# Kernel optimization log

Measured on AMD Instinct MI355X. Metric: run time of the kernel, lower is better.

The kernel has to match this reference:

```python
import jax, jax.numpy as jnp
import numpy as np

B, O, D = 4096, 256, 256  # batch, size_out (rules), size_in (features)


def setup_inputs() -> dict:
    key = jax.random.key(0)
    k1, k2, k3, k4, k5 = jax.random.split(key, 5)
    return {
        "x": jax.random.normal(k1, (B, D), dtype=jnp.float32),
        "scales": jax.random.normal(k2, (O, D), dtype=jnp.float32),
        # strict upper triangle holds the packed rot vectors (original inits them to zeros;
        # small values keep the quadratic form well conditioned)
        "rots": jax.random.normal(k3, (O, D, D), dtype=jnp.float32) * 0.02,
        "centroids": jax.random.normal(k4, (O, D, 1), dtype=jnp.float32),
        "b": jax.random.uniform(k5, (O,), dtype=jnp.float32, minval=0.5, maxval=1.5),
    }


def reference(x, scales, rots, centroids, b):
    # Build symmetric transform A[o] = diag(scales[o]) + triu(rots[o],1) + triu(rots[o],1)^T
    # (equivalent to the loop of diag_embed(r_i, i+1) + mirrored lower diagonal).
    upper = jnp.triu(rots, 1)                                   # [O,D,D]
    A = upper + jnp.swapaxes(upper, -1, -2)
    A = A + jnp.eye(D, dtype=scales.dtype) * scales[:, None, :]  # diag_embed(scales)
    # Augmented affine map: mul[o,i,b'] = A[o] @ x[b'] + centroid[o,i]; const row dropped
    # since only the first size_in rows feed the norm.
    y = jnp.einsum('bj,oij->boi', x, A) + centroids[..., 0][None, :, :]  # [B,O,D]
    rx = jnp.sqrt(jnp.sum(y * y, axis=-1))                      # L2 norm over D -> [B,O]
    return 1.0 / (1.0 + rx ** (2.0 * b))                        # bell membership [B,O]
```

## Files before the change

kernel.cpp:

```cpp
#include <hip/hip_runtime.h>
#include <cstdint>
#include <cmath>

#define Bn 4096
#define Dn 256
#define On 256

typedef __bf16 v8bf __attribute__((ext_vector_type(8)));
typedef float  v16f __attribute__((ext_vector_type(16)));
typedef unsigned short us8 __attribute__((ext_vector_type(8)));

__device__ __forceinline__ unsigned short f2bf(float f) {
    unsigned int u = __builtin_bit_cast(unsigned int, f);
    unsigned int r = (u + 0x7fffu + ((u >> 16) & 1u)) >> 16;
    return (unsigned short)r;
}

__device__ __forceinline__ void gl_lds16(const void* g, void* l) {
    __builtin_amdgcn_global_load_lds(
        (const __attribute__((address_space(1))) void*)(uintptr_t)g,
        (__attribute__((address_space(3))) void*)(uintptr_t)l, 16, 0, 0);
}

__global__ __launch_bounds__(256) void prep_x(const float* __restrict__ x,
                                              unsigned short* __restrict__ xbT) {
    __shared__ float t[64][68];
    const int tid = threadIdx.x;
    const int bb = blockIdx.x >> 2;
    const int kb = blockIdx.x & 3;
    const int b0 = bb * 64;
#pragma unroll
    for (int s = 0; s < 4; ++s) {
        const int idx = s * 256 + tid;
        const int r = idx >> 4, c4 = idx & 15;
        const float4 v = *(const float4*)(x + (size_t)(b0 + r) * Dn + kb * 64 + c4 * 4);
        *(float4*)&t[r][c4 * 4] = v;
    }
    __syncthreads();
    const int lane = tid & 63, wv = tid >> 6;
#pragma unroll
    for (int s = 0; s < 2; ++s) {
        const int kcl = s * 4 + wv;
        us8 u;
#pragma unroll
        for (int q = 0; q < 8; ++q) u[q] = f2bf(t[lane][kcl * 8 + q]);
        *(us8*)(xbT + ((size_t)(kb * 8 + kcl) * Bn + b0 + lane) * 8) = u;
    }
}

template <int TI, int TJ>
__device__ __forceinline__ void extract_pair(const float* T, v8bf (&af)[16],
                                             float sc, int wv, int lane) {
    const int l31 = lane & 31, hw = lane >> 5;
    const int half = wv & 1, grp = wv >> 1;
    if (TI == TJ) {
        if (grp == TI) {
            const int r = half * 32 + l31;
            const int mr = (r & 7) << 2;
#pragma unroll
            for (int kq = 0; kq < 4; ++kq) {
                us8 u;
#pragma unroll
                for (int q = 0; q < 8; ++q) {
                    const int c = kq * 16 + hw * 8 + q;
                    const float v = (r < c) ? T[r * 64 + (c ^ mr)]
                                  : ((r > c) ? T[c * 64 + (r ^ ((c & 7) << 2))]
                                             : sc);
                    u[q] = f2bf(v);
                }
                af[TI * 4 + kq] = __builtin_bit_cast(v8bf, u);
            }
        }
    } else {
        if (grp == TI) {
            const int r = half * 32 + l31;
            const int mr = (r & 7) << 2;
#pragma unroll
            for (int kq = 0; kq < 4; ++kq) {
                const int c0 = kq * 16 + hw * 8;
                const float4 a = *(const float4*)&T[r * 64 + (c0 ^ mr)];
                const float4 b = *(const float4*)&T[r * 64 + ((c0 + 4) ^ mr)];
                us8 u;
                u[0] = f2bf(a.x); u[1] = f2bf(a.y); u[2] = f2bf(a.z); u[3] = f2bf(a.w);
                u[4] = f2bf(b.x); u[5] = f2bf(b.y); u[6] = f2bf(b.z); u[7] = f2bf(b.w);
                af[TJ * 4 + kq] = __builtin_bit_cast(v8bf, u);
            }
        } else if (grp == TJ) {
            const int cL = half * 32 + l31;
#pragma unroll
            for (int kq = 0; kq < 4; ++kq) {
                us8 u;
#pragma unroll
                for (int q = 0; q < 8; ++q) {
                    const int rL = kq * 16 + hw * 8 + q;
                    u[q] = f2bf(T[rL * 64 + (cL ^ ((rL & 7) << 2))]);
                }
                af[TI * 4 + kq] = __builtin_bit_cast(v8bf, u);
            }
        }
    }
}

#define WAITV(N)                                              \
    do {                                                      \
        asm volatile("s_waitcnt vmcnt(" #N ")" ::: "memory"); \
        __builtin_amdgcn_sched_barrier(0);                    \
    } while (0)
#define LGKM0()                                               \
    do {                                                      \
        asm volatile("s_waitcnt lgkmcnt(0)" ::: "memory");    \
        __builtin_amdgcn_sched_barrier(0);                    \
    } while (0)
#define BARF()                                                \
    do {                                                      \
        __builtin_amdgcn_sched_barrier(0);                    \
        __builtin_amdgcn_s_barrier();                         \
        __builtin_amdgcn_sched_barrier(0);                    \
    } while (0)

#define STAGE_T(TIv, TJv, DST)                                               \
    do {                                                                     \
        const float* s_ = rbase + (TIv) * (64 * Dn) + (TJv) * 64;            \
        _Pragma("unroll")                                                    \
        for (int s = 0; s < 2; ++s) {                                        \
            const int idx = s * 512 + tid;                                   \
            const int r = idx >> 4, c4 = idx & 15;                           \
            gl_lds16(s_ + (size_t)r * Dn + ((c4 ^ (r & 7)) * 4),             \
                     (DST) + idx * 4);                                       \
        }                                                                    \
    } while (0)

#define STAGE_X(BUF)                                                         \
    do {                                                                     \
        _Pragma("unroll")                                                    \
        for (int s = 0; s < 2; ++s) {                                        \
            gl_lds16(px[s], &Xs[BUF][s * 512 + tid][0]);                     \
            px[s] += 256;                  \
        }                                                                    \
    } while (0)

__global__ __launch_bounds__(512, 4) void fuzzy_main(
    const float* __restrict__ rots, const float* __restrict__ scales,
    const unsigned short* __restrict__ xbT, const float* __restrict__ cent,
    const float* __restrict__ bvals, float* __restrict__ out) {
    __shared__ __align__(16) unsigned short Xs[4][1024][8];
    __shared__ float ssbuf[2][8][32];
    __shared__ float centL[Dn];

    const int tid  = threadIdx.x;
    const int lane = tid & 63;
    const int wv   = tid >> 6;
    const int l31  = lane & 31, hw = lane >> 5;
    const int Lb = blockIdx.x;
    const int o     = (Lb & 7) * 32 + ((Lb >> 3) & 31);
    const int bhalf = Lb >> 8;
    const int bh0   = bhalf * 2048;

    if (tid < Dn) centL[tid] = cent[o * Dn + tid];
    const float sc = scales[o * Dn + wv * 32 + l31];
    const float bv = bvals[o];

    WAITV(0);

    float* const S0 = (float*)&Xs[0][0][0];
    float* const S1 = (float*)&Xs[1][0][0];
    float* const S2 = (float*)&Xs[2][0][0];
    float* const S3 = (float*)&Xs[3][0][0];
    const float* const rbase = rots + ((size_t)o << 16);

    v8bf af[16];

    STAGE_T(0, 1, S0); STAGE_T(2, 3, S1);
    STAGE_T(0, 2, S2); STAGE_T(1, 3, S3);
    WAITV(4); BARF();
    extract_pair<0, 1>(S0, af, sc, wv, lane);
    extract_pair<2, 3>(S1, af, sc, wv, lane);
    LGKM0(); BARF();
    STAGE_T(0, 3, S0); STAGE_T(1, 2, S1);
    WAITV(4); BARF();
    extract_pair<0, 2>(S2, af, sc, wv, lane);
    extract_pair<1, 3>(S3, af, sc, wv, lane);
    LGKM0(); BARF();
    STAGE_T(0, 0, S2); STAGE_T(1, 1, S3);
    WAITV(4); BARF();
    extract_pair<0, 3>(S0, af, sc, wv, lane);
    extract_pair<1, 2>(S1, af, sc, wv, lane);
    LGKM0(); BARF();
    STAGE_T(2, 2, S0); STAGE_T(3, 3, S1);
    WAITV(4); BARF();
    extract_pair<0, 0>(S2, af, sc, wv, lane);
    extract_pair<1, 1>(S3, af, sc, wv, lane);
    LGKM0(); BARF();
    WAITV(0); BARF();
    extract_pair<2, 2>(S0, af, sc, wv, lane);
    extract_pair<3, 3>(S1, af, sc, wv, lane);
    LGKM0(); BARF();

    const unsigned short* px[2];
#pragma unroll
    for (int s = 0; s < 2; ++s) {
        const int idx = s * 512 + tid;
        px[s] = xbT + ((size_t)(idx >> 5) * Bn + bh0 + (idx & 31)) * 8;
    }

    STAGE_X(0); STAGE_X(1); STAGE_X(2);
    WAITV(4);
    LGKM0(); BARF();

    for (int t = 0; t < 64; ++t) {
        const int buf = t & 3;
        if (t <= 60) STAGE_X((t + 3) & 3);

        if (t >= 1 && lane < 4) {
            const int bl = wv * 4 + lane;
            float ssq = 0.f;
#pragma unroll
            for (int w = 0; w < 8; ++w) ssq += ssbuf[(t - 1) & 1][w][bl];
            out[(size_t)(bh0 + (t - 1) * 32 + bl) * On + o] =
                1.0f / (1.0f + exp2f(bv * log2f(ssq)));
        }

        v16f a0, a1;
#pragma unroll
        for (int rg = 0; rg < 16; ++rg) { a0[rg] = 0.f; a1[rg] = 0.f; }
        __builtin_amdgcn_s_setprio(1);
#pragma unroll
        for (int ks = 0; ks < 16; ++ks) {
            const v8bf xf = *(const v8bf*)&Xs[buf][(ks * 2 + hw) * 32 + l31][0];
            if (ks & 1)
                a1 = __builtin_amdgcn_mfma_f32_32x32x16_bf16(af[ks], xf, a1, 0, 0, 0);
            else
                a0 = __builtin_amdgcn_mfma_f32_32x32x16_bf16(af[ks], xf, a0, 0, 0, 0);
        }
        __builtin_amdgcn_s_setprio(0);

        {
            float v = 0.f;
#pragma unroll
            for (int g = 0; g < 4; ++g) {
                const float4 c4 = *(const float4*)&centL[wv * 32 + 8 * g + 4 * hw];
                float y;
                y = a0[g * 4 + 0] + a1[g * 4 + 0] + c4.x; v = fmaf(y, y, v);
                y = a0[g * 4 + 1] + a1[g * 4 + 1] + c4.y; v = fmaf(y, y, v);
                y = a0[g * 4 + 2] + a1[g * 4 + 2] + c4.z; v = fmaf(y, y, v);
                y = a0[g * 4 + 3] + a1[g * 4 + 3] + c4.w; v = fmaf(y, y, v);
            }
            v += __shfl_xor(v, 32);
            if (lane < 32) ssbuf[t & 1][wv][l31] = v;
        }

        if (t < 61)      WAITV(4);
        else if (t == 61) WAITV(2);
        else              WAITV(0);
        LGKM0(); BARF();
    }

    if (lane < 4) {
        const int bl = wv * 4 + lane;
        float ssq = 0.f;
#pragma unroll
        for (int w = 0; w < 8; ++w) ssq += ssbuf[1][w][bl];
        out[(size_t)(bh0 + 63 * 32 + bl) * On + o] =
            1.0f / (1.0f + exp2f(bv * log2f(ssq)));
    }
}

__global__ void fallback_kernel(const float* __restrict__ x, const float* __restrict__ scales,
                                const float* __restrict__ rots, const float* __restrict__ cent,
                                const float* __restrict__ bvals, float* __restrict__ out) {
    const int b = blockIdx.x * blockDim.x + threadIdx.x;
    const int o = blockIdx.y;
    if (b >= Bn) return;
    const float* R  = rots + (size_t)o * Dn * Dn;
    const float* xv = x + (size_t)b * Dn;
    float ss = 0.f;
    for (int i = 0; i < Dn; ++i) {
        float a = cent[o * Dn + i];
        for (int j = 0; j < Dn; ++j) {
            const float w = (j > i) ? R[i * Dn + j]
                          : ((j < i) ? R[j * Dn + i] : scales[o * Dn + i]);
            a += w * xv[j];
        }
        ss += a * a;
    }
    out[(size_t)b * On + o] = 1.f / (1.f + powf(ss, bvals[o]));
}

extern "C" void kernel_launch(void* const* d_in, const int* in_sizes, int n_in,
                              void* d_out, int out_size, void* d_ws, size_t ws_size,
                              hipStream_t stream) {
    const float* x         = (const float*)d_in[0];
    const float* scales    = (const float*)d_in[1];
    const float* rots      = (const float*)d_in[2];
    const float* centroids = (const float*)d_in[3];
    const float* bvals     = (const float*)d_in[4];
    float* out = (float*)d_out;

    const size_t needX = (size_t)Bn * Dn * sizeof(unsigned short);

    if (ws_size >= needX) {
        unsigned short* xbT = (unsigned short*)d_ws;
        prep_x<<<dim3(256), 256, 0, stream>>>(x, xbT);
        fuzzy_main<<<dim3(512), 512, 0, stream>>>(rots, scales, xbT, centroids, bvals, out);
    } else {
        fallback_kernel<<<dim3(Bn / 256, On), 256, 0, stream>>>(x, scales, rots, centroids,
                                                                bvals, out);
    }
}
```

Before: 232.3 us.

## Process two batch tiles per barrier and batch output epilogue every eight tiles

The main loop now handles two 32-row batch tiles per iteration, staging the next two X buffers at once and synchronizing only once per pair. Each tile uses a single MFMA accumulator chain instead of two interleaved ones. Per-tile sum-of-squares results go into an enlarged 8-slot LDS buffer, and the final bell-membership outputs are computed and written by 32 lanes per wave every eight tiles instead of 4 lanes per tile. The aim is to cut barrier and epilogue overhead, at the cost of a serial MFMA dependency chain, full vmcnt(0) waits that remove prefetch overlap, and an extra barrier in the periodic epilogue.

After: 226.8 us. 2.3% less time.

```diff
diff --git a/kernel.cpp b/kernel.cpp
--- a/kernel.cpp
+++ b/kernel.cpp
@@ -144,7 +144,7 @@
     const unsigned short* __restrict__ xbT, const float* __restrict__ cent,
     const float* __restrict__ bvals, float* __restrict__ out) {
     __shared__ __align__(16) unsigned short Xs[4][1024][8];
-    __shared__ float ssbuf[2][8][32];
+    __shared__ float ssbuf[8][8][32];
     __shared__ float centL[Dn];
 
     const int tid  = threadIdx.x;
@@ -203,65 +203,56 @@
         px[s] = xbT + ((size_t)(idx >> 5) * Bn + bh0 + (idx & 31)) * 8;
     }
 
-    STAGE_X(0); STAGE_X(1); STAGE_X(2);
-    WAITV(4);
-    LGKM0(); BARF();
-
-    for (int t = 0; t < 64; ++t) {
-        const int buf = t & 3;
-        if (t <= 60) STAGE_X((t + 3) & 3);
-
-        if (t >= 1 && lane < 4) {
-            const int bl = wv * 4 + lane;
-            float ssq = 0.f;
-#pragma unroll
-            for (int w = 0; w < 8; ++w) ssq += ssbuf[(t - 1) & 1][w][bl];
-            out[(size_t)(bh0 + (t - 1) * 32 + bl) * On + o] =
-                1.0f / (1.0f + exp2f(bv * log2f(ssq)));
-        }
-
-        v16f a0, a1;
-#pragma unroll
-        for (int rg = 0; rg < 16; ++rg) { a0[rg] = 0.f; a1[rg] = 0.f; }
-        __builtin_amdgcn_s_setprio(1);
-#pragma unroll
-        for (int ks = 0; ks < 16; ++ks) {
-            const v8bf xf = *(const v8bf*)&Xs[buf][(ks * 2 + hw) * 32 + l31][0];
-            if (ks & 1)
-                a1 = __builtin_amdgcn_mfma_f32_32x32x16_bf16(af[ks], xf, a1, 0, 0, 0);
-            else
-                a0 = __builtin_amdgcn_mfma_f32_32x32x16_bf16(af[ks], xf, a0, 0, 0, 0);
-        }
-        __builtin_amdgcn_s_setprio(0);
-
-        {
+    STAGE_X(0); STAGE_X(1);
+    WAITV(0); LGKM0(); BARF();
+
+    for (int p = 0; p < 32; ++p) {
+        const int t0 = 2 * p;
+        if (p < 31) { STAGE_X((t0 + 2) & 3); STAGE_X((t0 + 3) & 3); }
+
+#pragma unroll
+        for (int s = 0; s < 2; ++s) {
+            const int t = t0 + s;
+            const int buf = t & 3;
+
+            v16f a;
+#pragma unroll
+            for (int rg = 0; rg < 16; ++rg) a[rg] = 0.f;
+            __builtin_amdgcn_s_setprio(1);
+#pragma unroll
+            for (int ks = 0; ks < 16; ++ks) {
+                const v8bf xf = *(const v8bf*)&Xs[buf][(ks * 2 + hw) * 32 + l31][0];
+                a = __builtin_amdgcn_mfma_f32_32x32x16_bf16(af[ks], xf, a, 0, 0, 0);
+            }
+            __builtin_amdgcn_s_setprio(0);
+
             float v = 0.f;
 #pragma unroll
             for (int g = 0; g < 4; ++g) {
                 const float4 c4 = *(const float4*)&centL[wv * 32 + 8 * g + 4 * hw];
                 float y;
-                y = a0[g * 4 + 0] + a1[g * 4 + 0] + c4.x; v = fmaf(y, y, v);
-                y = a0[g * 4 + 1] + a1[g * 4 + 1] + c4.y; v = fmaf(y, y, v);
-                y = a0[g * 4 + 2] + a1[g * 4 + 2] + c4.z; v = fmaf(y, y, v);
-                y = a0[g * 4 + 3] + a1[g * 4 + 3] + c4.w; v = fmaf(y, y, v);
+                y = a[g * 4 + 0] + c4.x; v = fmaf(y, y, v);
+                y = a[g * 4 + 1] + c4.y; v = fmaf(y, y, v);
+                y = a[g * 4 + 2] + c4.z; v = fmaf(y, y, v);
+                y = a[g * 4 + 3] + c4.w; v = fmaf(y, y, v);
             }
             v += __shfl_xor(v, 32);
-            if (lane < 32) ssbuf[t & 1][wv][l31] = v;
-        }
-
-        if (t < 61)      WAITV(4);
-        else if (t == 61) WAITV(2);
-        else              WAITV(0);
-        LGKM0(); BARF();
-    }
-
-    if (lane < 4) {
-        const int bl = wv * 4 + lane;
-        float ssq = 0.f;
-#pragma unroll
-        for (int w = 0; w < 8; ++w) ssq += ssbuf[1][w][bl];
-        out[(size_t)(bh0 + 63 * 32 + bl) * On + o] =
-            1.0f / (1.0f + exp2f(bv * log2f(ssq)));
+            if (lane < 32) ssbuf[t & 7][wv][l31] = v;
+        }
+
+        WAITV(0); LGKM0(); BARF();
+
+        if ((p & 3) == 3) {
+            const int tb = (p >> 2) * 8 + wv;
+            if (lane < 32) {
+                float ssq = 0.f;
+#pragma unroll
+                for (int w2 = 0; w2 < 8; ++w2) ssq += ssbuf[wv][w2][l31];
+                out[(size_t)(bh0 + tb * 32 + l31) * On + o] =
+                    1.0f / (1.0f + exp2f(bv * log2f(ssq)));
+            }
+            LGKM0(); BARF();
+        }
     }
 }
 
```
